# Kernel optimization log

Measured on AMD Instinct MI355X. Metric: run time of the kernel, lower is better.

Reference implementation:

```python
import jax, jax.numpy as jnp
import numpy as np

B, T, H = 512, 256, 256


def setup_inputs() -> dict:
    key = jax.random.key(0)
    ks = jax.random.split(key, 12)
    s = 1.0 / np.sqrt(H)
    return {
        "h_tilde": jax.random.normal(ks[0], (B, H), jnp.float32),
        "c_t": jax.random.normal(ks[1], (B, H), jnp.float32),
        "h_history": jax.random.normal(ks[2], (B, T, H), jnp.float32),
        "deltaT_hist": jax.random.uniform(ks[3], (B, T, 1), jnp.float32),
        "deltaL_hist": jax.random.uniform(ks[4], (B, T, 1), jnp.float32),
        "W_I": jax.random.normal(ks[5], (H, 2 * H), jnp.float32) * s,
        "W_Ih": jax.random.normal(ks[6], (H, H), jnp.float32) * s,
        "W_I1T": jax.random.normal(ks[7], (H, 1), jnp.float32),
        "W_I1L": jax.random.normal(ks[8], (H, 1), jnp.float32),
        "b_I": jnp.zeros((H,), jnp.float32),
        "W_oI": jax.random.normal(ks[9], (H, H), jnp.float32) * s,
        "b_oI": jnp.zeros((H,), jnp.float32),
        "v_t": jax.random.normal(ks[10], (H,), jnp.float32),
    }


def reference(h_tilde, c_t, h_history, deltaT_hist, deltaL_hist,
              W_I, W_Ih, W_I1T, W_I1L, b_I, W_oI, b_oI, v_t):
    # h_hat: [B, 2H]; current projection: [B, H]
    h_hat = jnp.concatenate([h_tilde, c_t], axis=1)
    current_proj = h_hat @ W_I.T
    # Batched per-step additive attention pre-activation I_ti: [B, T, H]
    I = (current_proj[:, None, :]
         + jnp.einsum('bth,oh->bto', h_history, W_Ih)
         + deltaT_hist * W_I1T[:, 0]          # [B,T,1]*[H] -> [B,T,H]
         + deltaL_hist * W_I1L[:, 0]
         + b_I)
    o = jnp.tanh(jnp.einsum('bti,oi->bto', I, W_oI) + b_oI)  # [B, T, H]
    scores = jnp.einsum('bth,h->bt', o, v_t)                  # [B, T]
    alpha = jax.nn.softmax(scores, axis=1)
    s_t = jnp.einsum('bt,bth->bh', alpha, h_history)          # [B, H]
    return (s_t, alpha)
```

## Files before the change

### kernel.cpp

```cpp
#include <hip/hip_runtime.h>
#include <hip/hip_bf16.h>
#include <hip/hip_fp16.h>

#define Hdim 256
#define Tdim 256
#define Bdim 512
#define TT   64
#define NTILE (Tdim / TT)
#define NTHR 256
#define NCP  32

typedef __attribute__((ext_vector_type(8))) short s16x8;
typedef __attribute__((ext_vector_type(8))) _Float16 f16x8;
typedef __attribute__((ext_vector_type(2))) _Float16 f16x2;
typedef __attribute__((ext_vector_type(4))) float f32x4;
typedef unsigned short u16;
typedef unsigned int u32;

__device__ __forceinline__ u32 cvt_pk_f16(float lo, float hi) {
    auto v = __builtin_amdgcn_cvt_pkrtz(lo, hi);
    return __builtin_bit_cast(u32, v);
}
__device__ __forceinline__ u16 f2h_rne(float x) {
    _Float16 h = (_Float16)x;
    return __builtin_bit_cast(u16, h);
}
__device__ __forceinline__ f32x4 mfma16h(s16x8 a, s16x8 b, f32x4 c) {
    return __builtin_amdgcn_mfma_f32_16x16x32_f16(
        __builtin_bit_cast(f16x8, a), __builtin_bit_cast(f16x8, b), c, 0, 0, 0);
}
__device__ __forceinline__ float fast_tanh(float z) {
    float e = __expf(2.0f * z);
    return 1.0f - 2.0f * __builtin_amdgcn_rcpf(e + 1.0f);
}
__device__ __forceinline__ s16x8 bfrag_f32(const float* __restrict__ wp) {
    float4 x0 = *(const float4*)(wp + 0);
    float4 x1 = *(const float4*)(wp + 4);
    uint4 uu = make_uint4(cvt_pk_f16(x0.x, x0.y), cvt_pk_f16(x0.z, x0.w),
                          cvt_pk_f16(x1.x, x1.y), cvt_pk_f16(x1.z, x1.w));
    return __builtin_bit_cast(s16x8, uu);
}
__device__ __forceinline__ void gload_lds16(const void* g, void* l) {
    __builtin_amdgcn_global_load_lds(
        (const __attribute__((address_space(1))) unsigned int*)g,
        (__attribute__((address_space(3))) unsigned int*)l, 16, 0, 0);
}

__global__ __launch_bounds__(256) void prep_kernel(
        const float* __restrict__ W_Ih, const float* __restrict__ W_oI,
        const float* __restrict__ W_I1T, const float* __restrict__ W_I1L,
        const float* __restrict__ h_tilde, const float* __restrict__ c_t,
        const float* __restrict__ W_I, const float* __restrict__ b_I,
        const float* __restrict__ b_oI,
        u16* __restrict__ Wph, float* __restrict__ wT2, float* __restrict__ wL2,
        float* __restrict__ cp2) {
    __shared__ char smem[24576];
    __shared__ float redT[4], redL[4];
    const int tid = threadIdx.x;
    const int w = tid >> 6, lane = tid & 63;
    const int c = lane & 15, g = lane >> 4;

    if (blockIdx.x < Hdim) {
        float* sWo = (float*)smem;
        const int o = blockIdx.x;
        const int j = tid;
        sWo[j] = W_oI[o * Hdim + j];
        __syncthreads();
        float a0 = 0.f, a1 = 0.f, a2 = 0.f, a3 = 0.f;
        #pragma unroll 8
        for (int i = 0; i < Hdim; i += 4) {
            a0 += sWo[i + 0] * W_Ih[(i + 0) * Hdim + j];
            a1 += sWo[i + 1] * W_Ih[(i + 1) * Hdim + j];
            a2 += sWo[i + 2] * W_Ih[(i + 2) * Hdim + j];
            a3 += sWo[i + 3] * W_Ih[(i + 3) * Hdim + j];
        }
        const float acc = (a0 + a1) + (a2 + a3);
        const int dst = (o >> 4) * 4096 + (j >> 5) * 512 + ((j >> 3) & 3) * 128
                      + (o & 15) * 8 + (j & 7);
        Wph[dst] = f2h_rne(acc);
        float pT = sWo[j] * W_I1T[j];
        float pL = sWo[j] * W_I1L[j];
        #pragma unroll
        for (int d = 1; d < 64; d <<= 1) {
            pT += __shfl_xor(pT, d, 64);
            pL += __shfl_xor(pL, d, 64);
        }
        if (lane == 0) { redT[w] = pT; redL[w] = pL; }
        __syncthreads();
        if (j == 0) {
            wT2[o] = redT[0] + redT[1] + redT[2] + redT[3];
            wL2[o] = redL[0] + redL[1] + redL[2] + redL[3];
        }
    } else {
        char* hh_b  = smem;
        char* cpl_b = smem + 16384;
        const int b0 = (blockIdx.x - Hdim) * 16;
        const u32 swzA = (u32)((c & 7) << 4);
        const f32x4 fz = {0.f, 0.f, 0.f, 0.f};
        {
            const int srow = tid >> 4;
            const int sj = tid & 15;
            const u32 sbb = (u32)(srow * 1024);
            const u32 ssz = (u32)((srow & 7) << 4);
            #pragma unroll
            for (int ch = 0; ch < 2; ++ch) {
                const int col = sj * 32 + ch * 16;
                const float* src = (col < Hdim)
                    ? (h_tilde + (size_t)(b0 + srow) * Hdim + col)
                    : (c_t + (size_t)(b0 + srow) * Hdim + col - Hdim);
                float4 f0 = *(const float4*)(src + 0);
                float4 f1 = *(const float4*)(src + 4);
                float4 f2 = *(const float4*)(src + 8);
                float4 f3 = *(const float4*)(src + 12);
                uint4 ua = make_uint4(cvt_pk_f16(f0.x, f0.y), cvt_pk_f16(f0.z, f0.w),
                                      cvt_pk_f16(f1.x, f1.y), cvt_pk_f16(f1.z, f1.w));
                uint4 ub = make_uint4(cvt_pk_f16(f2.x, f2.y), cvt_pk_f16(f2.z, f2.w),
                                      cvt_pk_f16(f3.x, f3.y), cvt_pk_f16(f3.z, f3.w));
                *(uint4*)(hh_b + ((sbb + (u32)(col * 2) + 0) ^ ssz)) = ua;
                *(uint4*)(hh_b + ((sbb + (u32)(col * 2) + 16) ^ ssz)) = ub;
            }
        }
        __syncthreads();
        f32x4 acc[4];
        #pragma unroll
        for (int n = 0; n < 4; ++n) acc[n] = fz;
        #pragma unroll
        for (int ks = 0; ks < 16; ++ks) {
            const s16x8 a = *(const s16x8*)(hh_b +
                (((u32)(c * 1024 + ks * 64 + g * 16)) ^ swzA));
            #pragma unroll
            for (int n = 0; n < 4; ++n) {
                const int o = w * 64 + n * 16 + c;
                const s16x8 bf = bfrag_f32(W_I + (size_t)o * (2 * Hdim) + ks * 32 + g * 8);
                acc[n] = mfma16h(a, bf, acc[n]);
            }
        }
        #pragma unroll
        for (int n = 0; n < 4; ++n) {
            const int o = w * 64 + n * 16 + c;
            const float bi = b_I[o];
            const u32 ocol2 = (u32)((o & ~1) * 2);
            #pragma unroll
            for (int r = 0; r < 4; ++r) {
                const int row = g * 4 + r;
                float z = acc[n][r] + bi;
                float zsw = __shfl_xor(z, 1, 64);
                if (!(c & 1)) {
                    u32 h2 = cvt_pk_f16(z, zsw);
                    *(u32*)(cpl_b + (((u32)(row * 512) + ocol2) ^ ((u32)((row & 7) << 4)))) = h2;
                }
            }
        }
        __syncthreads();
        f32x4 acc2[4];
        #pragma unroll
        for (int n = 0; n < 4; ++n) acc2[n] = fz;
        #pragma unroll
        for (int ks = 0; ks < 8; ++ks) {
            const s16x8 a = *(const s16x8*)(cpl_b +
                (((u32)(c * 512 + ks * 64 + g * 16)) ^ swzA));
            #pragma unroll
            for (int n = 0; n < 4; ++n) {
                const int o = w * 64 + n * 16 + c;
                const s16x8 bf = bfrag_f32(W_oI + (size_t)o * Hdim + ks * 32 + g * 8);
                acc2[n] = mfma16h(a, bf, acc2[n]);
            }
        }
        #pragma unroll
        for (int n = 0; n < 4; ++n) {
            const int o = w * 64 + n * 16 + c;
            const float bo = b_oI[o];
            #pragma unroll
            for (int r = 0; r < 4; ++r)
                cp2[(size_t)(b0 + g * 4 + r) * Hdim + o] = acc2[n][r] + bo;
        }
    }
}

__global__ __launch_bounds__(NTHR) void scores_kernel(
        const float* __restrict__ hist, const float* __restrict__ dT,
        const float* __restrict__ dL, const float* __restrict__ cp2,
        const u16* __restrict__ Wph,
        const float* __restrict__ wT2, const float* __restrict__ wL2,
        const float* __restrict__ v_t, float* __restrict__ scores,
        float* __restrict__ Spart, float* __restrict__ mpart,
        float* __restrict__ lpart) {
    __shared__ float lds_f[TT * Hdim];
    __shared__ float dtl[TT], dll[TT];
    __shared__ float sc_part[4][TT];
    __shared__ float p_sh[TT];
    __shared__ float ml_sh[2];
    __shared__ float sacc2[2][Hdim];

    const int bid = blockIdx.x;
    const int b = bid >> 2;
    const int t0 = (bid & 3) * TT;
    const int tid = threadIdx.x;
    const int w = tid >> 6, lane = tid & 63;
    const int c = lane & 15, g = lane >> 4;
    const int ob = w * 64;

    const int wfrag = lane * 8;
    #define WOFF(n, ks) ((w * 4 + (n)) * 4096 + (ks) * 512 + wfrag)

    {
        const float* hrow = hist + ((size_t)b * Tdim + t0 + w * 16) * Hdim;
        char* lrow = (char*)lds_f + (w * 16) * 1024;
        const int goff = (int)((((lane >> 1) ^ 0) << 3) | ((lane & 1) << 2));
        #pragma unroll
        for (int i = 0; i < 16; ++i) {
            const int row7 = (w * 16 + i) & 7;
            const int gl = ((lane >> 1) ^ row7);
            gload_lds16(hrow + (size_t)i * Hdim + gl * 8 + (lane & 1) * 4,
                        lrow + i * 1024);
        }
        (void)goff;
    }
    if (tid < TT) {
        dtl[tid] = dT[b * Tdim + t0 + tid];
        dll[tid] = dL[b * Tdim + t0 + tid];
    }
    __syncthreads();

    const f32x4 fz = {0.f, 0.f, 0.f, 0.f};

    f32x4 acc[4][4];
    #pragma unroll
    for (int m = 0; m < 4; ++m)
        #pragma unroll
        for (int n = 0; n < 4; ++n) acc[m][n] = fz;
    {
        const char* hb = (const char*)lds_f;
        #pragma unroll
        for (int ks = 0; ks < 8; ++ks) {
            s16x8 a[4];
            #pragma unroll
            for (int m = 0; m < 4; ++m) {
                const u32 ad = (u32)((m * 16 + c) * 1024
                             + ((u32)((ks * 4 + g) ^ (c & 7)) << 5));
                float4 x0 = *(const float4*)(hb + ad);
                float4 x1 = *(const float4*)(hb + ad + 16);
                uint4 uu = make_uint4(cvt_pk_f16(x0.x, x0.y), cvt_pk_f16(x0.z, x0.w),
                                      cvt_pk_f16(x1.x, x1.y), cvt_pk_f16(x1.z, x1.w));
                a[m] = __builtin_bit_cast(s16x8, uu);
            }
            #pragma unroll
            for (int n = 0; n < 4; ++n) {
                const s16x8 bh = *(const s16x8*)(Wph + WOFF(n, ks));
                #pragma unroll
                for (int m = 0; m < 4; ++m)
                    acc[m][n] = mfma16h(a[m], bh, acc[m][n]);
            }
        }
    }

    float cpv[4], wtv[4], wlv[4], vvv[4];
    #pragma unroll
    for (int n = 0; n < 4; ++n) {
        const int o = ob + n * 16 + c;
        cpv[n] = cp2[(size_t)b * Hdim + o];
        wtv[n] = wT2[o];
        wlv[n] = wL2[o];
        vvv[n] = v_t[o];
    }
    #pragma unroll
    for (int m = 0; m < 4; ++m) {
        #pragma unroll
        for (int r = 0; r < 4; ++r) {
            const int row = m * 16 + g * 4 + r;
            const float dtr = dtl[row], dlr = dll[row];
            float s = 0.f;
            #pragma unroll
            for (int n = 0; n < 4; ++n) {
                float z = acc[m][n][r] + cpv[n] + dtr * wtv[n] + dlr * wlv[n];
                s += fast_tanh(z) * vvv[n];
            }
            s += __shfl_xor(s, 1, 64);
            s += __shfl_xor(s, 2, 64);
            s += __shfl_xor(s, 4, 64);
            s += __shfl_xor(s, 8, 64);
            if (c == 0) sc_part[w][row] = s;
        }
    }
    __syncthreads();

    if (tid < TT) {
        float s = sc_part[0][tid] + sc_part[1][tid] + sc_part[2][tid] + sc_part[3][tid];
        scores[b * Tdim + t0 + tid] = s;
        float mx = s;
        #pragma unroll
        for (int d = 1; d < 64; d <<= 1) mx = fmaxf(mx, __shfl_xor(mx, d, 64));
        float p = __expf(s - mx);
        float l = p;
        #pragma unroll
        for (int d = 1; d < 64; d <<= 1) l += __shfl_xor(l, d, 64);
        p_sh[tid] = p;
        if (tid == 0) { ml_sh[0] = mx; ml_sh[1] = l; }
    }
    __syncthreads();

    {
        const int half = tid >> 7;
        const int pp = tid & 127;
        const char* hb = (const char*)lds_f;
        float s0 = 0.f, s1 = 0.f;
        #pragma unroll 8
        for (int i = 0; i < 32; ++i) {
            const int t = half * 32 + i;
            const float pv = p_sh[t];
            const u32 ad = (u32)(t * 1024
                         + (((u32)((pp >> 2) ^ (t & 7)) << 5) | (u32)((pp & 3) * 8)));
            const float2 hv = *(const float2*)(hb + ad);
            s0 += pv * hv.x;
            s1 += pv * hv.y;
        }
        sacc2[half][2 * pp] = s0;
        sacc2[half][2 * pp + 1] = s1;
    }
    __syncthreads();
    Spart[(size_t)bid * Hdim + tid] = sacc2[0][tid] + sacc2[1][tid];
    if (tid == 0) { mpart[bid] = ml_sh[0]; lpart[bid] = ml_sh[1]; }
    #undef WOFF
}

__global__ __launch_bounds__(256) void combine_kernel(
        const float* __restrict__ Spart, const float* __restrict__ mpart,
        const float* __restrict__ lpart, float* __restrict__ out) {
    const int b = blockIdx.x;
    const int tid = threadIdx.x;
    __shared__ float fsh[4], inv_l_sh, m_sh;
    if (tid == 0) {
        const float m0 = mpart[4 * b + 0], m1 = mpart[4 * b + 1];
        const float m2 = mpart[4 * b + 2], m3 = mpart[4 * b + 3];
        const float m = fmaxf(fmaxf(m0, m1), fmaxf(m2, m3));
        const float f0 = __expf(m0 - m), f1 = __expf(m1 - m);
        const float f2 = __expf(m2 - m), f3 = __expf(m3 - m);
        const float l = f0 * lpart[4 * b + 0] + f1 * lpart[4 * b + 1]
                      + f2 * lpart[4 * b + 2] + f3 * lpart[4 * b + 3];
        fsh[0] = f0; fsh[1] = f1; fsh[2] = f2; fsh[3] = f3;
        inv_l_sh = 1.0f / l;
        m_sh = m;
    }
    __syncthreads();
    const float inv_l = inv_l_sh;
    const float S = fsh[0] * Spart[(size_t)(4 * b + 0) * Hdim + tid]
                  + fsh[1] * Spart[(size_t)(4 * b + 1) * Hdim + tid]
                  + fsh[2] * Spart[(size_t)(4 * b + 2) * Hdim + tid]
                  + fsh[3] * Spart[(size_t)(4 * b + 3) * Hdim + tid];
    out[b * Hdim + tid] = S * inv_l;
    float* scores = out + Bdim * Hdim;
    const float sc = scores[b * Tdim + tid];
    scores[b * Tdim + tid] = __expf(sc - m_sh) * inv_l;
}

extern "C" void kernel_launch(void* const* d_in, const int* in_sizes, int n_in,
                              void* d_out, int out_size, void* d_ws, size_t ws_size,
                              hipStream_t stream) {
    const float* h_tilde = (const float*)d_in[0];
    const float* c_t     = (const float*)d_in[1];
    const float* hist    = (const float*)d_in[2];
    const float* dT      = (const float*)d_in[3];
    const float* dL      = (const float*)d_in[4];
    const float* W_I     = (const float*)d_in[5];
    const float* W_Ih    = (const float*)d_in[6];
    const float* W_I1T   = (const float*)d_in[7];
    const float* W_I1L   = (const float*)d_in[8];
    const float* b_I     = (const float*)d_in[9];
    const float* W_oI    = (const float*)d_in[10];
    const float* b_oI    = (const float*)d_in[11];
    const float* v_t     = (const float*)d_in[12];
    float* out = (float*)d_out;

    char* ws = (char*)d_ws;
    u16* Wph     = (u16*)ws;
    float* cp2   = (float*)(ws + 131072);
    float* wT2   = (float*)(ws + 655360);
    float* wL2   = (float*)(ws + 656384);
    float* Spart = (float*)(ws + 657408);
    float* mpart = (float*)(ws + 657408 + 2097152);
    float* lpart = (float*)(ws + 657408 + 2105344);
    float* scores = out + Bdim * Hdim;

    prep_kernel<<<dim3(Hdim + NCP), dim3(256), 0, stream>>>(
        W_Ih, W_oI, W_I1T, W_I1L, h_tilde, c_t, W_I, b_I, b_oI,
        Wph, wT2, wL2, cp2);
    scores_kernel<<<dim3(Bdim * NTILE), dim3(NTHR), 0, stream>>>(
        hist, dT, dL, cp2, Wph, wT2, wL2, v_t, scores, Spart, mpart, lpart);
    combine_kernel<<<dim3(Bdim), dim3(256), 0, stream>>>(Spart, mpart, lpart, out);
}
```

Baseline: 89.70 us.

## Fuse scores and combine into one per-batch kernel with double-buffered tiles

Replaces the per-tile scores kernel and the separate combine kernel with a single kernel of 512 threads per batch row. The kernel walks the four T-tiles, staging the next history tile into a second LDS buffer while the current one is computed. The partial softmax statistics and weighted sums stay in LDS, so the Spart/mpart/lpart round trip through global memory and one kernel launch go away. In exchange it uses about 128KB+ of LDS per block, allowing only one block per CU, launches 4x fewer blocks, and adds several block-wide barriers per tile, which can serialise the work.

Result: slower. 100.8 us (+12.4%).

```diff
diff --git a/kernel.cpp b/kernel.cpp
--- a/kernel.cpp
+++ b/kernel.cpp
@@ -7,7 +7,7 @@
 #define Bdim 512
 #define TT   64
 #define NTILE (Tdim / TT)
-#define NTHR 256
+#define NTHR 512
 #define NCP  32
 
 typedef __attribute__((ext_vector_type(8))) short s16x8;
@@ -177,60 +177,76 @@
     }
 }
 
-__global__ __launch_bounds__(NTHR) void scores_kernel(
+__global__ __launch_bounds__(NTHR) void attn_fused(
         const float* __restrict__ hist, const float* __restrict__ dT,
         const float* __restrict__ dL, const float* __restrict__ cp2,
         const u16* __restrict__ Wph,
         const float* __restrict__ wT2, const float* __restrict__ wL2,
-        const float* __restrict__ v_t, float* __restrict__ scores,
-        float* __restrict__ Spart, float* __restrict__ mpart,
-        float* __restrict__ lpart) {
-    __shared__ float lds_f[TT * Hdim];
-    __shared__ float dtl[TT], dll[TT];
-    __shared__ float sc_part[4][TT];
+        const float* __restrict__ v_t, float* __restrict__ out) {
+    __shared__ float lds_f[2 * TT * Hdim];
+    __shared__ float dtA[Tdim], dlA[Tdim];
+    __shared__ float sc_part[8][TT];
     __shared__ float p_sh[TT];
-    __shared__ float ml_sh[2];
-    __shared__ float sacc2[2][Hdim];
-
-    const int bid = blockIdx.x;
-    const int b = bid >> 2;
-    const int t0 = (bid & 3) * TT;
+    __shared__ float sc_all[Tdim];
+    __shared__ float sacc4[4][Hdim];
+    __shared__ float Sp_sh[NTILE][Hdim];
+    __shared__ float msh[NTILE], lsh[NTILE];
+
+    const int b = blockIdx.x;
     const int tid = threadIdx.x;
     const int w = tid >> 6, lane = tid & 63;
     const int c = lane & 15, g = lane >> 4;
-    const int ob = w * 64;
+    const int ob = w * 32;
+    const int q = tid >> 7, pp = tid & 127;
 
     const int wfrag = lane * 8;
-    #define WOFF(n, ks) ((w * 4 + (n)) * 4096 + (ks) * 512 + wfrag)
-
-    {
-        const float* hrow = hist + ((size_t)b * Tdim + t0 + w * 16) * Hdim;
-        char* lrow = (char*)lds_f + (w * 16) * 1024;
-        const int goff = (int)((((lane >> 1) ^ 0) << 3) | ((lane & 1) << 2));
-        #pragma unroll
-        for (int i = 0; i < 16; ++i) {
-            const int row7 = (w * 16 + i) & 7;
-            const int gl = ((lane >> 1) ^ row7);
-            gload_lds16(hrow + (size_t)i * Hdim + gl * 8 + (lane & 1) * 4,
-                        lrow + i * 1024);
-        }
-        (void)goff;
-    }
-    if (tid < TT) {
-        dtl[tid] = dT[b * Tdim + t0 + tid];
-        dll[tid] = dL[b * Tdim + t0 + tid];
-    }
+    #define WOFF(n, ks) ((w * 2 + (n)) * 4096 + (ks) * 512 + wfrag)
+
+    float cpv[2], wtv[2], wlv[2], vvv[2];
+    #pragma unroll
+    for (int n = 0; n < 2; ++n) {
+        const int o = ob + n * 16 + c;
+        cpv[n] = cp2[(size_t)b * Hdim + o];
+        wtv[n] = wT2[o];
+        wlv[n] = wL2[o];
+        vvv[n] = v_t[o];
+    }
+    if (tid < Tdim) {
+        dtA[tid] = dT[b * Tdim + tid];
+        dlA[tid] = dL[b * Tdim + tid];
+    }
+
+    const float* hbase = hist + (size_t)b * Tdim * Hdim;
+    #define STAGE_TILE(tt, bufp)                                                   \
+        {                                                                          \
+            char* lb = (char*)(bufp);                                              \
+            _Pragma("unroll")                                                      \
+            for (int i = 0; i < 8; ++i) {                                          \
+                const int row = w * 8 + i;                                         \
+                const int gl = ((lane >> 1) ^ (row & 7));                          \
+                gload_lds16(hbase + (size_t)((tt) * TT + row) * Hdim               \
+                                  + gl * 8 + (lane & 1) * 4,                       \
+                            lb + row * 1024 + lane * 16);                          \
+            }                                                                      \
+        }
+
+    STAGE_TILE(0, lds_f);
     __syncthreads();
 
     const f32x4 fz = {0.f, 0.f, 0.f, 0.f};
 
-    f32x4 acc[4][4];
-    #pragma unroll
-    for (int m = 0; m < 4; ++m)
-        #pragma unroll
-        for (int n = 0; n < 4; ++n) acc[m][n] = fz;
-    {
-        const char* hb = (const char*)lds_f;
+    #pragma unroll 1
+    for (int tile = 0; tile < NTILE; ++tile) {
+        const int buf = tile & 1;
+        const int t0 = tile * TT;
+        const char* hb = (const char*)lds_f + buf * 65536;
+        float* nb = lds_f + (buf ^ 1) * (TT * Hdim);
+
+        if (tile + 1 < NTILE) STAGE_TILE(tile + 1, nb);
+
+        f32x4 acc[4][2];
+        #pragma unroll
+        for (int m = 0; m < 4; ++m) { acc[m][0] = fz; acc[m][1] = fz; }
         #pragma unroll
         for (int ks = 0; ks < 8; ++ks) {
             s16x8 a[4];
@@ -245,112 +261,88 @@
                 a[m] = __builtin_bit_cast(s16x8, uu);
             }
             #pragma unroll
-            for (int n = 0; n < 4; ++n) {
+            for (int n = 0; n < 2; ++n) {
                 const s16x8 bh = *(const s16x8*)(Wph + WOFF(n, ks));
                 #pragma unroll
                 for (int m = 0; m < 4; ++m)
                     acc[m][n] = mfma16h(a[m], bh, acc[m][n]);
             }
         }
-    }
-
-    float cpv[4], wtv[4], wlv[4], vvv[4];
-    #pragma unroll
-    for (int n = 0; n < 4; ++n) {
-        const int o = ob + n * 16 + c;
-        cpv[n] = cp2[(size_t)b * Hdim + o];
-        wtv[n] = wT2[o];
-        wlv[n] = wL2[o];
-        vvv[n] = v_t[o];
-    }
-    #pragma unroll
-    for (int m = 0; m < 4; ++m) {
-        #pragma unroll
-        for (int r = 0; r < 4; ++r) {
-            const int row = m * 16 + g * 4 + r;
-            const float dtr = dtl[row], dlr = dll[row];
+
+        #pragma unroll
+        for (int m = 0; m < 4; ++m) {
+            #pragma unroll
+            for (int r = 0; r < 4; ++r) {
+                const int row = m * 16 + g * 4 + r;
+                const float dtr = dtA[t0 + row], dlr = dlA[t0 + row];
+                float s = 0.f;
+                #pragma unroll
+                for (int n = 0; n < 2; ++n) {
+                    float z = acc[m][n][r] + cpv[n] + dtr * wtv[n] + dlr * wlv[n];
+                    s += fast_tanh(z) * vvv[n];
+                }
+                s += __shfl_xor(s, 1, 64);
+                s += __shfl_xor(s, 2, 64);
+                s += __shfl_xor(s, 4, 64);
+                s += __shfl_xor(s, 8, 64);
+                if (c == 0) sc_part[w][row] = s;
+            }
+        }
+        __syncthreads();
+
+        if (tid < TT) {
             float s = 0.f;
             #pragma unroll
-            for (int n = 0; n < 4; ++n) {
-                float z = acc[m][n][r] + cpv[n] + dtr * wtv[n] + dlr * wlv[n];
-                s += fast_tanh(z) * vvv[n];
-            }
-            s += __shfl_xor(s, 1, 64);
-            s += __shfl_xor(s, 2, 64);
-            s += __shfl_xor(s, 4, 64);
-            s += __shfl_xor(s, 8, 64);
-            if (c == 0) sc_part[w][row] = s;
-        }
-    }
-    __syncthreads();
-
-    if (tid < TT) {
-        float s = sc_part[0][tid] + sc_part[1][tid] + sc_part[2][tid] + sc_part[3][tid];
-        scores[b * Tdim + t0 + tid] = s;
-        float mx = s;
-        #pragma unroll
-        for (int d = 1; d < 64; d <<= 1) mx = fmaxf(mx, __shfl_xor(mx, d, 64));
-        float p = __expf(s - mx);
-        float l = p;
-        #pragma unroll
-        for (int d = 1; d < 64; d <<= 1) l += __shfl_xor(l, d, 64);
-        p_sh[tid] = p;
-        if (tid == 0) { ml_sh[0] = mx; ml_sh[1] = l; }
-    }
-    __syncthreads();
-
-    {
-        const int half = tid >> 7;
-        const int pp = tid & 127;
-        const char* hb = (const char*)lds_f;
-        float s0 = 0.f, s1 = 0.f;
-        #pragma unroll 8
-        for (int i = 0; i < 32; ++i) {
-            const int t = half * 32 + i;
-            const float pv = p_sh[t];
-            const u32 ad = (u32)(t * 1024
-                         + (((u32)((pp >> 2) ^ (t & 7)) << 5) | (u32)((pp & 3) * 8)));
-            const float2 hv = *(const float2*)(hb + ad);
-            s0 += pv * hv.x;
-            s1 += pv * hv.y;
-        }
-        sacc2[half][2 * pp] = s0;
-        sacc2[half][2 * pp + 1] = s1;
-    }
-    __syncthreads();
-    Spart[(size_t)bid * Hdim + tid] = sacc2[0][tid] + sacc2[1][tid];
-    if (tid == 0) { mpart[bid] = ml_sh[0]; lpart[bid] = ml_sh[1]; }
-    #undef WOFF
-}
-
-__global__ __launch_bounds__(256) void combine_kernel(
-        const float* __restrict__ Spart, const float* __restrict__ mpart,
-        const float* __restrict__ lpart, float* __restrict__ out) {
-    const int b = blockIdx.x;
-    const int tid = threadIdx.x;
-    __shared__ float fsh[4], inv_l_sh, m_sh;
-    if (tid == 0) {
-        const float m0 = mpart[4 * b + 0], m1 = mpart[4 * b + 1];
-        const float m2 = mpart[4 * b + 2], m3 = mpart[4 * b + 3];
+            for (int ww = 0; ww < 8; ++ww) s += sc_part[ww][tid];
+            sc_all[t0 + tid] = s;
+            float mx = s;
+            #pragma unroll
+            for (int d = 1; d < 64; d <<= 1) mx = fmaxf(mx, __shfl_xor(mx, d, 64));
+            float p = __expf(s - mx);
+            float l = p;
+            #pragma unroll
+            for (int d = 1; d < 64; d <<= 1) l += __shfl_xor(l, d, 64);
+            p_sh[tid] = p;
+            if (tid == 0) { msh[tile] = mx; lsh[tile] = l; }
+        }
+        __syncthreads();
+
+        {
+            float s0 = 0.f, s1 = 0.f;
+            #pragma unroll 8
+            for (int i = 0; i < 16; ++i) {
+                const int t = q * 16 + i;
+                const float pv = p_sh[t];
+                const u32 ad = (u32)(t * 1024
+                             + (((u32)((pp >> 2) ^ (t & 7)) << 5) | (u32)((pp & 3) * 8)));
+                const float2 hv = *(const float2*)(hb + ad);
+                s0 += pv * hv.x;
+                s1 += pv * hv.y;
+            }
+            sacc4[q][2 * pp] = s0;
+            sacc4[q][2 * pp + 1] = s1;
+        }
+        __syncthreads();
+        if (tid < Hdim)
+            Sp_sh[tile][tid] = sacc4[0][tid] + sacc4[1][tid]
+                             + sacc4[2][tid] + sacc4[3][tid];
+        __syncthreads();
+    }
+
+    if (tid < Hdim) {
+        const float m0 = msh[0], m1 = msh[1], m2 = msh[2], m3 = msh[3];
         const float m = fmaxf(fmaxf(m0, m1), fmaxf(m2, m3));
         const float f0 = __expf(m0 - m), f1 = __expf(m1 - m);
         const float f2 = __expf(m2 - m), f3 = __expf(m3 - m);
-        const float l = f0 * lpart[4 * b + 0] + f1 * lpart[4 * b + 1]
-                      + f2 * lpart[4 * b + 2] + f3 * lpart[4 * b + 3];
-        fsh[0] = f0; fsh[1] = f1; fsh[2] = f2; fsh[3] = f3;
-        inv_l_sh = 1.0f / l;
-        m_sh = m;
-    }
-    __syncthreads();
-    const float inv_l = inv_l_sh;
-    const float S = fsh[0] * Spart[(size_t)(4 * b + 0) * Hdim + tid]
-                  + fsh[1] * Spart[(size_t)(4 * b + 1) * Hdim + tid]
-                  + fsh[2] * Spart[(size_t)(4 * b + 2) * Hdim + tid]
-                  + fsh[3] * Spart[(size_t)(4 * b + 3) * Hdim + tid];
-    out[b * Hdim + tid] = S * inv_l;
-    float* scores = out + Bdim * Hdim;
-    const float sc = scores[b * Tdim + tid];
-    scores[b * Tdim + tid] = __expf(sc - m_sh) * inv_l;
+        const float l = f0 * lsh[0] + f1 * lsh[1] + f2 * lsh[2] + f3 * lsh[3];
+        const float inv_l = 1.0f / l;
+        const float S = f0 * Sp_sh[0][tid] + f1 * Sp_sh[1][tid]
+                      + f2 * Sp_sh[2][tid] + f3 * Sp_sh[3][tid];
+        out[b * Hdim + tid] = S * inv_l;
+        out[Bdim * Hdim + b * Tdim + tid] = __expf(sc_all[tid] - m) * inv_l;
+    }
+    #undef WOFF
+    #undef STAGE_TILE
 }
 
 extern "C" void kernel_launch(void* const* d_in, const int* in_sizes, int n_in,
@@ -372,19 +364,14 @@
     float* out = (float*)d_out;
 
     char* ws = (char*)d_ws;
-    u16* Wph     = (u16*)ws;
-    float* cp2   = (float*)(ws + 131072);
-    float* wT2   = (float*)(ws + 655360);
-    float* wL2   = (float*)(ws + 656384);
-    float* Spart = (float*)(ws + 657408);
-    float* mpart = (float*)(ws + 657408 + 2097152);
-    float* lpart = (float*)(ws + 657408 + 2105344);
-    float* scores = out + Bdim * Hdim;
+    u16* Wph   = (u16*)ws;
+    float* cp2 = (float*)(ws + 131072);
+    float* wT2 = (float*)(ws + 655360);
+    float* wL2 = (float*)(ws + 656384);
 
     prep_kernel<<<dim3(Hdim + NCP), dim3(256), 0, stream>>>(
         W_Ih, W_oI, W_I1T, W_I1L, h_tilde, c_t, W_I, b_I, b_oI,
         Wph, wT2, wL2, cp2);
-    scores_kernel<<<dim3(Bdim * NTILE), dim3(NTHR), 0, stream>>>(
-        hist, dT, dL, cp2, Wph, wT2, wL2, v_t, scores, Spart, mpart, lpart);
-    combine_kernel<<<dim3(Bdim), dim3(256), 0, stream>>>(Spart, mpart, lpart, out);
-}
+    attn_fused<<<dim3(Bdim), dim3(NTHR), 0, stream>>>(
+        hist, dT, dL, cp2, Wph, wT2, wL2, v_t, out);
+}
```
